# Performance work log

Measured on AMD Instinct MI355X. Metric: run time of the kernel, lower is better.

The kernel has to match this reference:

```python
import jax, jax.numpy as jnp
import numpy as np

# NF4 16-level codebook (bitsandbytes values)
NF4_CODEBOOK = jnp.array([
    -1.0, -0.6961928009986877, -0.5250730514526367, -0.39491748809814453,
    -0.28444138169288635, -0.18477343022823334, -0.09105003625154495, 0.0,
    0.07958029955625534, 0.16093020141124725, 0.24611230194568634,
    0.33791524171829224, 0.44070982933044434, 0.5626170039176941,
    0.7229568362236328, 1.0], dtype=jnp.float32)

GROUP = 64      # quant_group_size for NF4
R = 16          # LoRA rank
ALPHA = 16      # lora_alpha -> scaling = ALPHA / R = 1.0
E, H, I, T, TOPK = 8, 2048, 1024, 512, 2


def nf4_dequant_gkn(packed, scales, K, N):
    """packed: [E, K//2, N] uint8-valued ints (two 4-bit codes per byte along K).
    scales: [E, K//GROUP, N] float32 per-group absmax. Returns [E, K, N] fp32."""
    e = packed.shape[0]
    lo = packed & 15
    hi = (packed >> 4) & 15
    codes = jnp.stack([lo, hi], axis=2).reshape(e, K, N)      # interleave along K
    w = NF4_CODEBOOK[codes]                                    # [E, K, N]
    w = w.reshape(e, K // GROUP, GROUP, N) * scales[:, :, None, :]
    return w.reshape(e, K, N)


def setup_inputs() -> dict:
    key = jax.random.key(0)
    ks = jax.random.split(key, 16)
    lora_std = 1.0 / np.sqrt(H)
    return {
        "x": jax.random.normal(ks[0], (T, H), jnp.float32),
        "topk_idx": jax.random.randint(ks[1], (T, TOPK), 0, E, jnp.int32),
        "topk_w": jax.random.uniform(ks[2], (T, TOPK), jnp.float32),
        "gate_packed": jax.random.randint(ks[3], (E, H // 2, I), 0, 256, jnp.int32),
        "gate_scales": jax.random.uniform(ks[4], (E, H // GROUP, I), jnp.float32) * 0.02,
        "up_packed": jax.random.randint(ks[5], (E, H // 2, I), 0, 256, jnp.int32),
        "up_scales": jax.random.uniform(ks[6], (E, H // GROUP, I), jnp.float32) * 0.02,
        "down_packed": jax.random.randint(ks[7], (E, I // 2, H), 0, 256, jnp.int32),
        "down_scales": jax.random.uniform(ks[8], (E, I // GROUP, H), jnp.float32) * 0.02,
        "gate_A": jax.random.normal(ks[9], (E, H, R), jnp.float32) * lora_std,
        "gate_B": jax.random.normal(ks[10], (E, R, I), jnp.float32) * 0.02,
        "up_A": jax.random.normal(ks[11], (E, H, R), jnp.float32) * lora_std,
        "up_B": jax.random.normal(ks[12], (E, R, I), jnp.float32) * 0.02,
        "down_A": jax.random.normal(ks[13], (E, I, R), jnp.float32) * lora_std,
        "down_B": jax.random.normal(ks[14], (E, R, H), jnp.float32) * 0.02,
    }


def reference(x, topk_idx, topk_w, gate_packed, gate_scales, up_packed, up_scales,
              down_packed, down_scales, gate_A, gate_B, up_A, up_B, down_A, down_B):
    scaling = ALPHA / R
    # Dequantized NF4 base + LoRA delta, GKN layout [E, K, N]
    Wg = nf4_dequant_gkn(gate_packed, gate_scales, H, I) + scaling * jnp.einsum('ekr,ern->ekn', gate_A, gate_B)
    Wu = nf4_dequant_gkn(up_packed, up_scales, H, I) + scaling * jnp.einsum('ekr,ern->ekn', up_A, up_B)
    Wd = nf4_dequant_gkn(down_packed, down_scales, I, H) + scaling * jnp.einsum('ekr,ern->ekn', down_A, down_B)
    # Grouped GEMM (dense-over-experts reference): SwiGLU per expert
    g = jnp.einsum('th,ehi->eti', x, Wg)          # [E, T, I]
    u = jnp.einsum('th,ehi->eti', x, Wu)
    h = jax.nn.silu(g) * u
    o = jnp.einsum('eti,eih->eth', h, Wd)         # [E, T, H]
    # Routing combine: per-token per-expert weight from top-k assignments
    w_te = jnp.sum((topk_idx[:, :, None] == jnp.arange(E)) * topk_w[:, :, None], axis=1)  # [T, E]
    return jnp.einsum('eth,te->th', o, w_te)
```

## Files before the change

### kernel.cpp

```cpp
#include <hip/hip_runtime.h>
#include <math.h>

#define NE 8
#define NH 2048
#define NI 1024
#define NT 512
#define NTOPK 2
#define NR 16
#define NGROUP 64
#define NPAIR (NT*NTOPK)

typedef short bf16x8 __attribute__((ext_vector_type(8)));
typedef float f32x16 __attribute__((ext_vector_type(16)));
typedef unsigned int u32;

#define MFMA32 __builtin_amdgcn_mfma_f32_32x32x16_bf16

__device__ const float NF4_TAB[16] = {
    -1.0f, -0.6961928009986877f, -0.5250730514526367f, -0.39491748809814453f,
    -0.28444138169288635f, -0.18477343022823334f, -0.09105003625154495f, 0.0f,
    0.07958029955625534f, 0.16093020141124725f, 0.24611230194568634f,
    0.33791524171829224f, 0.44070982933044434f, 0.5626170039176941f,
    0.7229568362236328f, 1.0f};

#define OFF_EXPOFF 0
#define OFF_TOK    256
#define OFF_EXP    4352
#define OFF_W      8448
#define OFF_XAG    12544
#define OFF_XAU    45312
#define OFF_HA     78080
#define OFF_XB     131072
#define OFF_GU     2228224
#define OFF_HBUF   6422528

__device__ inline u32 f2bf(float f) {
    return (__float_as_uint(f) + 0x8000u) >> 16;
}
__device__ inline u32 bfpack2(float a, float b) {
    return ((__float_as_uint(a) + 0x8000u) >> 16) |
           ((__float_as_uint(b) + 0x8000u) & 0xFFFF0000u);
}
__device__ inline bf16x8 asbf(uint4 w) {
    union { uint4 u; bf16x8 b; } c; c.u = w; return c.b;
}
__device__ inline bf16x8 bfzero() { return asbf(make_uint4(0,0,0,0)); }
__device__ inline float bf2f(u32 v) { return __uint_as_float(v << 16); }

__device__ __forceinline__ void stage16(const void* g, void* l) {
    __builtin_amdgcn_global_load_lds(
        (const __attribute__((address_space(1))) u32*)g,
        (__attribute__((address_space(3))) u32*)l, 16, 0, 0);
}

#define WAITV8()  asm volatile("s_waitcnt vmcnt(8)" ::: "memory")
#define WAITV0()  asm volatile("s_waitcnt vmcnt(0)" ::: "memory")

__global__ __launch_bounds__(1024) void k_route(const int* __restrict__ idx,
                                                const float* __restrict__ w,
                                                int* expert_off, int* ptok,
                                                int* pexp, float* pw) {
    __shared__ int cnt[NE], off[NE + 1], cur[NE];
    int tid = threadIdx.x;
    if (tid < NE) cnt[tid] = 0;
    __syncthreads();
    int e = idx[tid];
    float wt = w[tid];
    int t = tid >> 1;
    atomicAdd(&cnt[e], 1);
    __syncthreads();
    if (tid == 0) {
        off[0] = 0;
        for (int i = 0; i < NE; i++) off[i + 1] = off[i] + cnt[i];
    }
    __syncthreads();
    if (tid < NE) cur[tid] = off[tid];
    __syncthreads();
    int pos = atomicAdd(&cur[e], 1);
    ptok[pos] = t; pexp[pos] = e; pw[pos] = wt;
    if (tid <= NE) expert_off[tid] = off[tid];
}

__global__ __launch_bounds__(256) void k_xcvt(const float* __restrict__ x,
                                              unsigned short* __restrict__ xb) {
    int i = (blockIdx.x * 256 + threadIdx.x) * 8;
    float4 v0 = *(const float4*)(x + i);
    float4 v1 = *(const float4*)(x + i + 4);
    uint4 w;
    w.x = bfpack2(v0.x, v0.y); w.y = bfpack2(v0.z, v0.w);
    w.z = bfpack2(v1.x, v1.y); w.w = bfpack2(v1.z, v1.w);
    *(uint4*)(xb + i) = w;
}

__global__ __launch_bounds__(256) void k_xA(const float* __restrict__ x,
                                            const float* __restrict__ gA,
                                            const float* __restrict__ uA,
                                            const int* __restrict__ ptok,
                                            const int* __restrict__ pexp,
                                            unsigned short* __restrict__ xAg,
                                            unsigned short* __restrict__ xAu) {
    int p = blockIdx.x;
    int t = ptok[p], e = pexp[p];
    int tid = threadIdx.x;
    int r = tid & 15, ch = tid >> 4;
    const float* xr = x + (size_t)t * NH;
    const float* gAr = gA + (size_t)e * NH * NR;
    const float* uAr = uA + (size_t)e * NH * NR;
    float sg = 0.f, su = 0.f;
    for (int j = ch * 128; j < ch * 128 + 128; ++j) {
        float xv = xr[j];
        sg += xv * gAr[j * NR + r];
        su += xv * uAr[j * NR + r];
    }
    __shared__ float red[2][16][16];
    red[0][ch][r] = sg; red[1][ch][r] = su;
    __syncthreads();
    for (int st = 8; st >= 1; st >>= 1) {
        if (ch < st) {
            red[0][ch][r] += red[0][ch + st][r];
            red[1][ch][r] += red[1][ch + st][r];
        }
        __syncthreads();
    }
    if (tid < 16) {
        xAg[p * NR + tid] = (unsigned short)f2bf(red[0][0][tid]);
        xAu[p * NR + tid] = (unsigned short)f2bf(red[1][0][tid]);
    }
}

__global__ __launch_bounds__(64, 3) void k_gu(
    const unsigned short* __restrict__ xb,
    const int* __restrict__ gpk, const float* __restrict__ gsc,
    const int* __restrict__ upk, const float* __restrict__ usc,
    const float* __restrict__ gB, const float* __restrict__ uB,
    const unsigned short* __restrict__ xAg, const unsigned short* __restrict__ xAu,
    const int* __restrict__ expert_off, const int* __restrict__ ptok,
    unsigned short* __restrict__ gu)
{
    __shared__ u32 lut[256];
    __shared__ u32 code0[1024];
    __shared__ u32 code1[1024];
    __shared__ float sclb[32][32];

    int lane = threadIdx.x;
    int q = lane >> 5, cw = lane & 31;
    for (int i = lane; i < 256; i += 64)
        lut[i] = bfpack2(NF4_TAB[i & 15], NF4_TAB[(i >> 4) & 15]);

    int e = blockIdx.x;
    int c0 = blockIdx.y * 32;
    int mat = blockIdx.z & 1;
    int rt = blockIdx.z >> 1;
    const u32* pk = (const u32*)(mat ? upk : gpk);
    const float* scp = mat ? usc : gsc;
    const float* Bp = mat ? uB : gB;
    const unsigned short* xA = mat ? xAu : xAg;

    int off = expert_off[e];
    int cnt = expert_off[e + 1] - off;
    int colg = c0 + cw;
    const size_t pkb = (size_t)e * (NH / 2) * NI;

    {
        const float* sg = scp + (size_t)e * (NH / NGROUP) * NI + c0;
        #pragma unroll
        for (int g = 0; g < 4; ++g)
            stage16(sg + (size_t)(g * 8 + (lane >> 3)) * NI + ((lane & 7) << 2),
                    &sclb[g * 8][0]);
    }

    const int NS = NH / 64;
    for (int s0 = rt * 32; s0 < cnt; s0 += 128) {
        int rr = s0 + cw; if (rr > cnt - 1) rr = cnt - 1;
        u32 ro = (u32)ptok[off + rr] * (u32)NH;
        const unsigned short* xr = xb + ro + (q << 3);

        auto stageC = [&](u32* cb, int s) {
            int kp0 = s << 5;
            #pragma unroll
            for (int g = 0; g < 4; ++g)
                stage16(pk + pkb + (size_t)(kp0 + (g << 3) + (lane >> 3)) * NI
                            + c0 + ((lane & 7) << 2),
                        cb + (g << 8));
        };
        auto loadA = [&](bf16x8* d, int s) {
            #pragma unroll
            for (int ks = 0; ks < 4; ++ks)
                d[ks] = *(const bf16x8*)(xr + (s << 6) + (ks << 4));
        };

        bf16x8 Aa[4], Ab[4];
        f32x16 acc;
        #pragma unroll
        for (int i = 0; i < 16; ++i) acc[i] = 0.f;

        auto compute = [&](const u32* cb, const bf16x8* Ar, float scl) {
            f32x16 t;
            #pragma unroll
            for (int i = 0; i < 16; ++i) t[i] = 0.f;
            #pragma unroll
            for (int ks = 0; ks < 4; ++ks) {
                uint4 w4; u32* wp = &w4.x;
                #pragma unroll
                for (int i = 0; i < 4; ++i)
                    wp[i] = lut[cb[(((ks << 3) + (q << 2) + i) << 5) + cw] & 255];
                t = MFMA32(Ar[ks], asbf(w4), t, 0, 0, 0);
            }
            #pragma unroll
            for (int i = 0; i < 16; ++i) acc[i] += scl * t[i];
        };

        stageC(code0, 0); loadA(Aa, 0);
        stageC(code1, 1); loadA(Ab, 1);
        for (int s = 0; s < NS; s += 2) {
            WAITV8();
            compute(code0, Aa, sclb[s][cw]);
            if (s + 2 < NS) { stageC(code0, s + 2); loadA(Aa, s + 2); }
            if (s + 3 < NS) WAITV8(); else WAITV0();
            compute(code1, Ab, sclb[s + 1][cw]);
            if (s + 3 < NS) { stageC(code1, s + 3); loadA(Ab, s + 3); }
        }

        {
            bf16x8 la = bfzero();
            if (s0 + cw < cnt)
                la = *(const bf16x8*)(xA + (size_t)(off + s0 + cw) * NR + (q << 3));
            const float* Bq = Bp + ((size_t)e * NR + (q << 3)) * NI + colg;
            uint4 w4; u32* wp = &w4.x;
            #pragma unroll
            for (int i = 0; i < 4; ++i)
                wp[i] = bfpack2(Bq[(2 * i) * NI], Bq[(2 * i + 1) * NI]);
            acc = MFMA32(la, asbf(w4), acc, 0, 0, 0);
        }
        unsigned short* outb = gu + (size_t)mat * NPAIR * NI;
        #pragma unroll
        for (int reg = 0; reg < 16; ++reg) {
            int rloc = (reg & 3) + 8 * (reg >> 2) + (q << 2);
            if (s0 + rloc < cnt)
                outb[(size_t)(off + s0 + rloc) * NI + colg] =
                    (unsigned short)f2bf(acc[reg]);
        }
    }
}

__global__ __launch_bounds__(256) void k_swiglu(const unsigned short* __restrict__ gu,
                                                unsigned short* __restrict__ hbuf) {
    int i = (blockIdx.x * 256 + threadIdx.x) * 8;
    uint4 gv = *(const uint4*)(gu + i);
    uint4 uv = *(const uint4*)(gu + (size_t)NPAIR * NI + i);
    const u32* gp = &gv.x; const u32* up = &uv.x;
    uint4 hv; u32* hp = &hv.x;
    #pragma unroll
    for (int j = 0; j < 4; ++j) {
        float g0 = bf2f(gp[j] & 0xFFFFu), g1 = bf2f(gp[j] >> 16);
        float u0 = bf2f(up[j] & 0xFFFFu), u1 = bf2f(up[j] >> 16);
        float h0 = g0 * u0 / (1.f + __expf(-g0));
        float h1 = g1 * u1 / (1.f + __expf(-g1));
        hp[j] = bfpack2(h0, h1);
    }
    *(uint4*)(hbuf + i) = hv;
}

__global__ __launch_bounds__(256) void k_hA(const unsigned short* __restrict__ hbuf,
                                            const float* __restrict__ dA,
                                            const int* __restrict__ pexp,
                                            unsigned short* __restrict__ hA) {
    int p = blockIdx.x;
    int e = pexp[p];
    int tid = threadIdx.x;
    int r = tid & 15, ch = tid >> 4;
    const unsigned short* hr = hbuf + (size_t)p * NI;
    const float* dAr = dA + (size_t)e * NI * NR;
    float sv = 0.f;
    for (int j = ch * 64; j < ch * 64 + 64; ++j) {
        float hv = bf2f(hr[j]);
        sv += hv * dAr[j * NR + r];
    }
    __shared__ float red[16][16];
    red[ch][r] = sv;
    __syncthreads();
    for (int st = 8; st >= 1; st >>= 1) {
        if (ch < st) red[ch][r] += red[ch + st][r];
        __syncthreads();
    }
    if (tid < 16) hA[p * NR + tid] = (unsigned short)f2bf(red[0][tid]);
}

__global__ __launch_bounds__(64, 3) void k_dn(
    const unsigned short* __restrict__ hbuf,
    const int* __restrict__ dpk, const float* __restrict__ dsc,
    const float* __restrict__ dB,
    const unsigned short* __restrict__ hA,
    const int* __restrict__ expert_off, const int* __restrict__ ptok,
    const float* __restrict__ pw,
    float* __restrict__ out)
{
    __shared__ u32 lut[256];
    __shared__ u32 code0[1024];
    __shared__ u32 code1[1024];
    __shared__ float sclb[16][32];

    int lane = threadIdx.x;
    int q = lane >> 5, cw = lane & 31;
    for (int i = lane; i < 256; i += 64)
        lut[i] = bfpack2(NF4_TAB[i & 15], NF4_TAB[(i >> 4) & 15]);

    int e = blockIdx.x;
    int c0 = blockIdx.y * 32;
    int rt = blockIdx.z;
    const u32* pk = (const u32*)dpk;

    int off = expert_off[e];
    int cnt = expert_off[e + 1] - off;
    int colg = c0 + cw;
    const size_t pkb = (size_t)e * (NI / 2) * NH;

    {
        const float* sg = dsc + (size_t)e * (NI / NGROUP) * NH + c0;
        #pragma unroll
        for (int g = 0; g < 2; ++g)
            stage16(sg + (size_t)(g * 8 + (lane >> 3)) * NH + ((lane & 7) << 2),
                    &sclb[g * 8][0]);
    }

    const int NS = NI / 64;
    for (int s0 = rt * 32; s0 < cnt; s0 += 128) {
        int rr = s0 + cw; if (rr > cnt - 1) rr = cnt - 1;
        u32 ro = (u32)(off + rr) * (u32)NI;
        const unsigned short* hr = hbuf + ro + (q << 3);

        auto stageC = [&](u32* cb, int s) {
            int kp0 = s << 5;
            #pragma unroll
            for (int g = 0; g < 4; ++g)
                stage16(pk + pkb + (size_t)(kp0 + (g << 3) + (lane >> 3)) * NH
                            + c0 + ((lane & 7) << 2),
                        cb + (g << 8));
        };
        auto loadA = [&](bf16x8* d, int s) {
            #pragma unroll
            for (int ks = 0; ks < 4; ++ks)
                d[ks] = *(const bf16x8*)(hr + (s << 6) + (ks << 4));
        };

        bf16x8 Aa[4], Ab[4];
        f32x16 acc;
        #pragma unroll
        for (int i = 0; i < 16; ++i) acc[i] = 0.f;

        auto compute = [&](const u32* cb, const bf16x8* Ar, float scl) {
            f32x16 t;
            #pragma unroll
            for (int i = 0; i < 16; ++i) t[i] = 0.f;
            #pragma unroll
            for (int ks = 0; ks < 4; ++ks) {
                uint4 w4; u32* wp = &w4.x;
                #pragma unroll
                for (int i = 0; i < 4; ++i)
                    wp[i] = lut[cb[(((ks << 3) + (q << 2) + i) << 5) + cw] & 255];
                t = MFMA32(Ar[ks], asbf(w4), t, 0, 0, 0);
            }
            #pragma unroll
            for (int i = 0; i < 16; ++i) acc[i] += scl * t[i];
        };

        stageC(code0, 0); loadA(Aa, 0);
        stageC(code1, 1); loadA(Ab, 1);
        for (int s = 0; s < NS; s += 2) {
            WAITV8();
            compute(code0, Aa, sclb[s][cw]);
            if (s + 2 < NS) { stageC(code0, s + 2); loadA(Aa, s + 2); }
            if (s + 3 < NS) WAITV8(); else WAITV0();
            compute(code1, Ab, sclb[s + 1][cw]);
            if (s + 3 < NS) { stageC(code1, s + 3); loadA(Ab, s + 3); }
        }

        {
            bf16x8 la = bfzero();
            if (s0 + cw < cnt)
                la = *(const bf16x8*)(hA + (size_t)(off + s0 + cw) * NR + (q << 3));
            const float* Bq = dB + ((size_t)e * NR + (q << 3)) * NH + colg;
            uint4 w4; u32* wp = &w4.x;
            #pragma unroll
            for (int i = 0; i < 4; ++i)
                wp[i] = bfpack2(Bq[(2 * i) * NH], Bq[(2 * i + 1) * NH]);
            acc = MFMA32(la, asbf(w4), acc, 0, 0, 0);
        }
        #pragma unroll
        for (int reg = 0; reg < 16; ++reg) {
            int rloc = (reg & 3) + 8 * (reg >> 2) + (q << 2);
            if (s0 + rloc < cnt) {
                int p = off + s0 + rloc;
                atomicAdd(&out[(size_t)ptok[p] * NH + colg], acc[reg] * pw[p]);
            }
        }
    }
}

extern "C" void kernel_launch(void* const* d_in, const int* in_sizes, int n_in,
                              void* d_out, int out_size, void* d_ws,
                              size_t ws_size, hipStream_t stream) {
    const float* x = (const float*)d_in[0];
    const int* topk_idx = (const int*)d_in[1];
    const float* topk_w = (const float*)d_in[2];
    const int* gate_packed = (const int*)d_in[3];
    const float* gate_scales = (const float*)d_in[4];
    const int* up_packed = (const int*)d_in[5];
    const float* up_scales = (const float*)d_in[6];
    const int* down_packed = (const int*)d_in[7];
    const float* down_scales = (const float*)d_in[8];
    const float* gate_A = (const float*)d_in[9];
    const float* gate_B = (const float*)d_in[10];
    const float* up_A = (const float*)d_in[11];
    const float* up_B = (const float*)d_in[12];
    const float* down_A = (const float*)d_in[13];
    const float* down_B = (const float*)d_in[14];
    float* out = (float*)d_out;

    char* ws = (char*)d_ws;
    int* expert_off = (int*)(ws + OFF_EXPOFF);
    int* ptok = (int*)(ws + OFF_TOK);
    int* pexp = (int*)(ws + OFF_EXP);
    float* pw = (float*)(ws + OFF_W);
    unsigned short* xAg = (unsigned short*)(ws + OFF_XAG);
    unsigned short* xAu = (unsigned short*)(ws + OFF_XAU);
    unsigned short* hA = (unsigned short*)(ws + OFF_HA);
    unsigned short* xb = (unsigned short*)(ws + OFF_XB);
    unsigned short* gu = (unsigned short*)(ws + OFF_GU);
    unsigned short* hbuf = (unsigned short*)(ws + OFF_HBUF);

    hipMemsetAsync(d_out, 0, (size_t)NT * NH * sizeof(float), stream);

    k_route<<<1, 1024, 0, stream>>>(topk_idx, topk_w, expert_off, ptok, pexp, pw);
    k_xcvt<<<(NT * NH) / (256 * 8), 256, 0, stream>>>(x, xb);
    k_xA<<<NPAIR, 256, 0, stream>>>(x, gate_A, up_A, ptok, pexp, xAg, xAu);
    k_gu<<<dim3(NE, NI / 32, 8), 64, 0, stream>>>(
        xb, gate_packed, gate_scales, up_packed, up_scales, gate_B, up_B,
        xAg, xAu, expert_off, ptok, gu);
    k_swiglu<<<(NPAIR * NI) / (256 * 8), 256, 0, stream>>>(gu, hbuf);
    k_hA<<<NPAIR, 256, 0, stream>>>(hbuf, down_A, pexp, hA);
    k_dn<<<dim3(NE, NH / 32, 4), 64, 0, stream>>>(
        hbuf, down_packed, down_scales, down_B, hA, expert_off, ptok, pw, out);
}
```

Before: 275.0 us.

## Gather tokens into k-chunk-major activations and load NF4 codes directly to registers

Replaces the dense bf16 copy of x with a per-pair gathered buffer laid out k-chunk-major, so the activation loads in the grouped GEMMs are contiguous across rows. The swiglu output h gets the same transposed layout. The packed NF4 codes are now loaded per lane straight into registers instead of staged through LDS with global_load_lds and explicit vmcnt waits. This drops LDS traffic and the manual wait scheme but relies on the compiler to schedule the register prefetch. The code loads are scalar 4-byte reads strided by the row pitch, and k_hA now reads h with a strided access pattern.

After: 490.8 us. +78.5%, slower.

```diff
diff --git a/kernel.cpp b/kernel.cpp
--- a/kernel.cpp
+++ b/kernel.cpp
@@ -30,9 +30,9 @@
 #define OFF_XAG    12544
 #define OFF_XAU    45312
 #define OFF_HA     78080
-#define OFF_XB     131072
-#define OFF_GU     2228224
-#define OFF_HBUF   6422528
+#define OFF_XCT    131072
+#define OFF_GU     4325376
+#define OFF_HT     8519680
 
 __device__ inline u32 f2bf(float f) {
     return (__float_as_uint(f) + 0x8000u) >> 16;
@@ -52,9 +52,6 @@
         (const __attribute__((address_space(1))) u32*)g,
         (__attribute__((address_space(3))) u32*)l, 16, 0, 0);
 }
-
-#define WAITV8()  asm volatile("s_waitcnt vmcnt(8)" ::: "memory")
-#define WAITV0()  asm volatile("s_waitcnt vmcnt(0)" ::: "memory")
 
 __global__ __launch_bounds__(1024) void k_route(const int* __restrict__ idx,
                                                 const float* __restrict__ w,
@@ -81,15 +78,19 @@
     if (tid <= NE) expert_off[tid] = off[tid];
 }
 
-__global__ __launch_bounds__(256) void k_xcvt(const float* __restrict__ x,
-                                              unsigned short* __restrict__ xb) {
-    int i = (blockIdx.x * 256 + threadIdx.x) * 8;
-    float4 v0 = *(const float4*)(x + i);
-    float4 v1 = *(const float4*)(x + i + 4);
+__global__ __launch_bounds__(256) void k_xg(const float* __restrict__ x,
+                                            const int* __restrict__ ptok,
+                                            unsigned short* __restrict__ xcT) {
+    int p = blockIdx.x;
+    int t = ptok[p];
+    int k = threadIdx.x * 8;
+    const float* xr = x + (size_t)t * NH + k;
+    float4 v0 = *(const float4*)xr;
+    float4 v1 = *(const float4*)(xr + 4);
     uint4 w;
     w.x = bfpack2(v0.x, v0.y); w.y = bfpack2(v0.z, v0.w);
     w.z = bfpack2(v1.x, v1.y); w.w = bfpack2(v1.z, v1.w);
-    *(uint4*)(xb + i) = w;
+    *(uint4*)(xcT + ((size_t)(k >> 3) * NPAIR + p) * 8) = w;
 }
 
 __global__ __launch_bounds__(256) void k_xA(const float* __restrict__ x,
@@ -129,17 +130,15 @@
 }
 
 __global__ __launch_bounds__(64, 3) void k_gu(
-    const unsigned short* __restrict__ xb,
+    const unsigned short* __restrict__ xcT,
     const int* __restrict__ gpk, const float* __restrict__ gsc,
     const int* __restrict__ upk, const float* __restrict__ usc,
     const float* __restrict__ gB, const float* __restrict__ uB,
     const unsigned short* __restrict__ xAg, const unsigned short* __restrict__ xAu,
-    const int* __restrict__ expert_off, const int* __restrict__ ptok,
+    const int* __restrict__ expert_off,
     unsigned short* __restrict__ gu)
 {
     __shared__ u32 lut[256];
-    __shared__ u32 code0[1024];
-    __shared__ u32 code1[1024];
     __shared__ float sclb[32][32];
 
     int lane = threadIdx.x;
@@ -168,57 +167,65 @@
             stage16(sg + (size_t)(g * 8 + (lane >> 3)) * NI + ((lane & 7) << 2),
                     &sclb[g * 8][0]);
     }
+    asm volatile("s_waitcnt vmcnt(0)" ::: "memory");
+
+    const u32* pkc = pk + pkb + (size_t)(q << 2) * NI + colg;
 
     const int NS = NH / 64;
     for (int s0 = rt * 32; s0 < cnt; s0 += 128) {
         int rr = s0 + cw; if (rr > cnt - 1) rr = cnt - 1;
-        u32 ro = (u32)ptok[off + rr] * (u32)NH;
-        const unsigned short* xr = xb + ro + (q << 3);
-
-        auto stageC = [&](u32* cb, int s) {
-            int kp0 = s << 5;
-            #pragma unroll
-            for (int g = 0; g < 4; ++g)
-                stage16(pk + pkb + (size_t)(kp0 + (g << 3) + (lane >> 3)) * NI
-                            + c0 + ((lane & 7) << 2),
-                        cb + (g << 8));
+        int prow = off + rr;
+        const unsigned short* xr = xcT + ((size_t)q * NPAIR + prow) * 8;
+
+        auto loadC = [&](uint4* cb, int s) {
+            const u32* bb = pkc + (size_t)(s << 5) * NI;
+            #pragma unroll
+            for (int ks = 0; ks < 4; ++ks) {
+                uint4 c;
+                c.x = bb[(size_t)((ks << 3) + 0) * NI];
+                c.y = bb[(size_t)((ks << 3) + 1) * NI];
+                c.z = bb[(size_t)((ks << 3) + 2) * NI];
+                c.w = bb[(size_t)((ks << 3) + 3) * NI];
+                cb[ks] = c;
+            }
         };
         auto loadA = [&](bf16x8* d, int s) {
             #pragma unroll
             for (int ks = 0; ks < 4; ++ks)
-                d[ks] = *(const bf16x8*)(xr + (s << 6) + (ks << 4));
-        };
-
+                d[ks] = *(const bf16x8*)(xr +
+                            (size_t)((s << 3) + (ks << 1)) * NPAIR * 8);
+        };
+
+        uint4 Ca[4], Cb[4];
         bf16x8 Aa[4], Ab[4];
         f32x16 acc;
         #pragma unroll
         for (int i = 0; i < 16; ++i) acc[i] = 0.f;
 
-        auto compute = [&](const u32* cb, const bf16x8* Ar, float scl) {
+        auto compute = [&](const uint4* cb, const bf16x8* Ar, float scl) {
             f32x16 t;
             #pragma unroll
             for (int i = 0; i < 16; ++i) t[i] = 0.f;
             #pragma unroll
             for (int ks = 0; ks < 4; ++ks) {
-                uint4 w4; u32* wp = &w4.x;
-                #pragma unroll
-                for (int i = 0; i < 4; ++i)
-                    wp[i] = lut[cb[(((ks << 3) + (q << 2) + i) << 5) + cw] & 255];
+                uint4 w4;
+                w4.x = lut[cb[ks].x & 255];
+                w4.y = lut[cb[ks].y & 255];
+                w4.z = lut[cb[ks].z & 255];
+                w4.w = lut[cb[ks].w & 255];
                 t = MFMA32(Ar[ks], asbf(w4), t, 0, 0, 0);
             }
             #pragma unroll
             for (int i = 0; i < 16; ++i) acc[i] += scl * t[i];
         };
 
-        stageC(code0, 0); loadA(Aa, 0);
-        stageC(code1, 1); loadA(Ab, 1);
+        loadC(Ca, 0); loadA(Aa, 0);
+        loadC(Cb, 1); loadA(Ab, 1);
         for (int s = 0; s < NS; s += 2) {
-            WAITV8();
-            compute(code0, Aa, sclb[s][cw]);
-            if (s + 2 < NS) { stageC(code0, s + 2); loadA(Aa, s + 2); }
-            if (s + 3 < NS) WAITV8(); else WAITV0();
-            compute(code1, Ab, sclb[s + 1][cw]);
-            if (s + 3 < NS) { stageC(code1, s + 3); loadA(Ab, s + 3); }
+            compute(Ca, Aa, sclb[s][cw]);
+            if (s + 2 < NS) { loadC(Ca, s + 2); loadA(Aa, s + 2); }
+            compute(Cb, Ab, sclb[s + 1][cw]);
+            if (s + 3 < NS) { loadC(Cb, s + 3); loadA(Ab, s + 3); }
         }
 
         {
@@ -244,8 +251,10 @@
 }
 
 __global__ __launch_bounds__(256) void k_swiglu(const unsigned short* __restrict__ gu,
-                                                unsigned short* __restrict__ hbuf) {
+                                                unsigned short* __restrict__ hT) {
     int i = (blockIdx.x * 256 + threadIdx.x) * 8;
+    int p = i >> 10;
+    int k0 = i & 1023;
     uint4 gv = *(const uint4*)(gu + i);
     uint4 uv = *(const uint4*)(gu + (size_t)NPAIR * NI + i);
     const u32* gp = &gv.x; const u32* up = &uv.x;
@@ -258,10 +267,10 @@
         float h1 = g1 * u1 / (1.f + __expf(-g1));
         hp[j] = bfpack2(h0, h1);
     }
-    *(uint4*)(hbuf + i) = hv;
-}
-
-__global__ __launch_bounds__(256) void k_hA(const unsigned short* __restrict__ hbuf,
+    *(uint4*)(hT + ((size_t)(k0 >> 3) * NPAIR + p) * 8) = hv;
+}
+
+__global__ __launch_bounds__(256) void k_hA(const unsigned short* __restrict__ hT,
                                             const float* __restrict__ dA,
                                             const int* __restrict__ pexp,
                                             unsigned short* __restrict__ hA) {
@@ -269,11 +278,10 @@
     int e = pexp[p];
     int tid = threadIdx.x;
     int r = tid & 15, ch = tid >> 4;
-    const unsigned short* hr = hbuf + (size_t)p * NI;
     const float* dAr = dA + (size_t)e * NI * NR;
     float sv = 0.f;
     for (int j = ch * 64; j < ch * 64 + 64; ++j) {
-        float hv = bf2f(hr[j]);
+        float hv = bf2f(hT[((size_t)(j >> 3) * NPAIR + p) * 8 + (j & 7)]);
         sv += hv * dAr[j * NR + r];
     }
     __shared__ float red[16][16];
@@ -287,7 +295,7 @@
 }
 
 __global__ __launch_bounds__(64, 3) void k_dn(
-    const unsigned short* __restrict__ hbuf,
+    const unsigned short* __restrict__ hT,
     const int* __restrict__ dpk, const float* __restrict__ dsc,
     const float* __restrict__ dB,
     const unsigned short* __restrict__ hA,
@@ -296,8 +304,6 @@
     float* __restrict__ out)
 {
     __shared__ u32 lut[256];
-    __shared__ u32 code0[1024];
-    __shared__ u32 code1[1024];
     __shared__ float sclb[16][32];
 
     int lane = threadIdx.x;
@@ -322,57 +328,65 @@
             stage16(sg + (size_t)(g * 8 + (lane >> 3)) * NH + ((lane & 7) << 2),
                     &sclb[g * 8][0]);
     }
+    asm volatile("s_waitcnt vmcnt(0)" ::: "memory");
+
+    const u32* pkc = pk + pkb + (size_t)(q << 2) * NH + colg;
 
     const int NS = NI / 64;
     for (int s0 = rt * 32; s0 < cnt; s0 += 128) {
         int rr = s0 + cw; if (rr > cnt - 1) rr = cnt - 1;
-        u32 ro = (u32)(off + rr) * (u32)NI;
-        const unsigned short* hr = hbuf + ro + (q << 3);
-
-        auto stageC = [&](u32* cb, int s) {
-            int kp0 = s << 5;
-            #pragma unroll
-            for (int g = 0; g < 4; ++g)
-                stage16(pk + pkb + (size_t)(kp0 + (g << 3) + (lane >> 3)) * NH
-                            + c0 + ((lane & 7) << 2),
-                        cb + (g << 8));
+        int prow = off + rr;
+        const unsigned short* hr = hT + ((size_t)q * NPAIR + prow) * 8;
+
+        auto loadC = [&](uint4* cb, int s) {
+            const u32* bb = pkc + (size_t)(s << 5) * NH;
+            #pragma unroll
+            for (int ks = 0; ks < 4; ++ks) {
+                uint4 c;
+                c.x = bb[(size_t)((ks << 3) + 0) * NH];
+                c.y = bb[(size_t)((ks << 3) + 1) * NH];
+                c.z = bb[(size_t)((ks << 3) + 2) * NH];
+                c.w = bb[(size_t)((ks << 3) + 3) * NH];
+                cb[ks] = c;
+            }
         };
         auto loadA = [&](bf16x8* d, int s) {
             #pragma unroll
             for (int ks = 0; ks < 4; ++ks)
-                d[ks] = *(const bf16x8*)(hr + (s << 6) + (ks << 4));
-        };
-
+                d[ks] = *(const bf16x8*)(hr +
+                            (size_t)((s << 3) + (ks << 1)) * NPAIR * 8);
+        };
+
+        uint4 Ca[4], Cb[4];
         bf16x8 Aa[4], Ab[4];
         f32x16 acc;
         #pragma unroll
         for (int i = 0; i < 16; ++i) acc[i] = 0.f;
 
-        auto compute = [&](const u32* cb, const bf16x8* Ar, float scl) {
+        auto compute = [&](const uint4* cb, const bf16x8* Ar, float scl) {
             f32x16 t;
             #pragma unroll
             for (int i = 0; i < 16; ++i) t[i] = 0.f;
             #pragma unroll
             for (int ks = 0; ks < 4; ++ks) {
-                uint4 w4; u32* wp = &w4.x;
-                #pragma unroll
-                for (int i = 0; i < 4; ++i)
-                    wp[i] = lut[cb[(((ks << 3) + (q << 2) + i) << 5) + cw] & 255];
+                uint4 w4;
+                w4.x = lut[cb[ks].x & 255];
+                w4.y = lut[cb[ks].y & 255];
+                w4.z = lut[cb[ks].z & 255];
+                w4.w = lut[cb[ks].w & 255];
                 t = MFMA32(Ar[ks], asbf(w4), t, 0, 0, 0);
             }
             #pragma unroll
             for (int i = 0; i < 16; ++i) acc[i] += scl * t[i];
         };
 
-        stageC(code0, 0); loadA(Aa, 0);
-        stageC(code1, 1); loadA(Ab, 1);
+        loadC(Ca, 0); loadA(Aa, 0);
+        loadC(Cb, 1); loadA(Ab, 1);
         for (int s = 0; s < NS; s += 2) {
-            WAITV8();
-            compute(code0, Aa, sclb[s][cw]);
-            if (s + 2 < NS) { stageC(code0, s + 2); loadA(Aa, s + 2); }
-            if (s + 3 < NS) WAITV8(); else WAITV0();
-            compute(code1, Ab, sclb[s + 1][cw]);
-            if (s + 3 < NS) { stageC(code1, s + 3); loadA(Ab, s + 3); }
+            compute(Ca, Aa, sclb[s][cw]);
+            if (s + 2 < NS) { loadC(Ca, s + 2); loadA(Aa, s + 2); }
+            compute(Cb, Ab, sclb[s + 1][cw]);
+            if (s + 3 < NS) { loadC(Cb, s + 3); loadA(Ab, s + 3); }
         }
 
         {
@@ -425,20 +439,20 @@
     unsigned short* xAg = (unsigned short*)(ws + OFF_XAG);
     unsigned short* xAu = (unsigned short*)(ws + OFF_XAU);
     unsigned short* hA = (unsigned short*)(ws + OFF_HA);
-    unsigned short* xb = (unsigned short*)(ws + OFF_XB);
+    unsigned short* xcT = (unsigned short*)(ws + OFF_XCT);
     unsigned short* gu = (unsigned short*)(ws + OFF_GU);
-    unsigned short* hbuf = (unsigned short*)(ws + OFF_HBUF);
+    unsigned short* hT = (unsigned short*)(ws + OFF_HT);
 
     hipMemsetAsync(d_out, 0, (size_t)NT * NH * sizeof(float), stream);
 
     k_route<<<1, 1024, 0, stream>>>(topk_idx, topk_w, expert_off, ptok, pexp, pw);
-    k_xcvt<<<(NT * NH) / (256 * 8), 256, 0, stream>>>(x, xb);
+    k_xg<<<NPAIR, 256, 0, stream>>>(x, ptok, xcT);
     k_xA<<<NPAIR, 256, 0, stream>>>(x, gate_A, up_A, ptok, pexp, xAg, xAu);
     k_gu<<<dim3(NE, NI / 32, 8), 64, 0, stream>>>(
-        xb, gate_packed, gate_scales, up_packed, up_scales, gate_B, up_B,
-        xAg, xAu, expert_off, ptok, gu);
-    k_swiglu<<<(NPAIR * NI) / (256 * 8), 256, 0, stream>>>(gu, hbuf);
-    k_hA<<<NPAIR, 256, 0, stream>>>(hbuf, down_A, pexp, hA);
+        xcT, gate_packed, gate_scales, up_packed, up_scales, gate_B, up_B,
+        xAg, xAu, expert_off, gu);
+    k_swiglu<<<(NPAIR * NI) / (256 * 8), 256, 0, stream>>>(gu, hT);
+    k_hA<<<NPAIR, 256, 0, stream>>>(hT, down_A, pexp, hA);
     k_dn<<<dim3(NE, NH / 32, 4), 64, 0, stream>>>(
-        hbuf, down_packed, down_scales, down_B, hA, expert_off, ptok, pw, out);
-}
+        hT, down_packed, down_scales, down_B, hA, expert_off, ptok, pw, out);
+}
```
